# Optimization experiments

Hardware: AMD Instinct MI355X
Metric: run time of the kernel (lower is better)

## Reference

```python
import jax, jax.numpy as jnp
import numpy as np

IN_SIZE = 64
OUT_SIZE = 64
H1 = 2
H2 = 2
BATCH = 8192


def setup_inputs() -> dict:
    key = jax.random.key(0)
    ks = jax.random.split(key, 8)
    x = jax.random.normal(ks[0], (BATCH, IN_SIZE), dtype=jnp.float32)
    # Per-connection tiny MLP params; grid of (In, Out) subnets.
    # Layer 1: Linear(1, H1) -> w1:[In,Out,H1], b1:[In,Out,H1]
    # Layer 2: Linear(H1, H2) -> w2:[In,Out,H2,H1], b2:[In,Out,H2]
    # Layer 3: Linear(H2, 1) -> w3:[In,Out,H2], b3:[In,Out]
    s1 = 1.0  # kaiming-ish scale for fan_in=1
    s2 = 1.0 / np.sqrt(H1)
    s3 = 1.0 / np.sqrt(H2)
    w1 = jax.random.uniform(ks[1], (IN_SIZE, OUT_SIZE, H1), jnp.float32, -s1, s1)
    b1 = jax.random.uniform(ks[2], (IN_SIZE, OUT_SIZE, H1), jnp.float32, -s1, s1)
    w2 = jax.random.uniform(ks[3], (IN_SIZE, OUT_SIZE, H2, H1), jnp.float32, -s2, s2)
    b2 = jax.random.uniform(ks[4], (IN_SIZE, OUT_SIZE, H2), jnp.float32, -s2, s2)
    w3 = jax.random.uniform(ks[5], (IN_SIZE, OUT_SIZE, H2), jnp.float32, -s3, s3)
    b3 = jax.random.uniform(ks[6], (IN_SIZE, OUT_SIZE), jnp.float32, -s3, s3)
    return {"x": x, "w1": w1, "b1": b1, "w2": w2, "b2": b2, "w3": w3, "b3": b3}


def reference(x, w1, b1, w2, b2, w3, b3):
    # x: [B, In]. Each (in, out) connection has its own tiny 3-layer MLP on a scalar.
    # h1: [B, In, Out, H1] = relu(x * w1 + b1)  (input dim is 1, so it's a scale)
    h1 = jax.nn.relu(x[:, :, None, None] * w1[None] + b1[None])
    # h2: [B, In, Out, H2]
    h2 = jax.nn.relu(jnp.einsum('bioh,iokh->biok', h1, w2) + b2[None])
    # scalar output per connection: [B, In, Out]
    y = jnp.einsum('biok,iok->bio', h2, w3) + b3[None]
    # KAN combination: sum contributions over inputs -> [B, Out]
    return jnp.sum(y, axis=1)
```

## Files before the change

kernel.cpp:

```cpp
#include <hip/hip_runtime.h>


#define IN_SIZE  64
#define OUT_SIZE 64
#define BATCH    8192

constexpr int WAVES   = 16;
constexpr int I_CHUNK = 4;
constexpr int BT      = 32;
constexpr int RG      = 8;
constexpr int PAD     = 17;

__device__ __forceinline__ void pin(float& v) {
    asm volatile("" : "+v"(v));
}

__device__ __forceinline__ void conn(float xv, float2 W1, float2 B1,
                                     float4 W2, float2 B2, float2 W3,
                                     float& s) {
    const float h0 = fmaxf(fmaf(xv, W1.x, B1.x), 0.f);
    const float h1 = fmaxf(fmaf(xv, W1.y, B1.y), 0.f);
    float u0 = fmaf(h1, W2.y, fmaf(h0, W2.x, B2.x));
    float u1 = fmaf(h1, W2.w, fmaf(h0, W2.z, B2.y));
    u0 = fmaxf(u0, 0.f);
    u1 = fmaxf(u1, 0.f);
    s = fmaf(u0, W3.x, s);
    s = fmaf(u1, W3.y, s);
}

__global__ __launch_bounds__(1024, 4) void kan_kernel(
    const float* __restrict__ x,
    const float* __restrict__ w1, const float* __restrict__ b1,
    const float* __restrict__ w2, const float* __restrict__ b2,
    const float* __restrict__ w3, const float* __restrict__ b3,
    float* __restrict__ out)
{
    const int tid   = threadIdx.x;
    const int o     = tid & 63;
    const int wv    = tid >> 6;
    const int brow0 = blockIdx.x * BT;

    __shared__ float xs[BT * IN_SIZE];
    __shared__ float ps[RG * OUT_SIZE * PAD];

    {
        const float2* xg = reinterpret_cast<const float2*>(x + brow0 * IN_SIZE);
        reinterpret_cast<float2*>(xs)[tid] = xg[tid];
    }

    const int i0 = wv * I_CHUNK;
    float2 W1[I_CHUNK], B1[I_CHUNK], B2[I_CHUNK], W3[I_CHUNK];
    float4 W2[I_CHUNK];
    float bacc = 0.f;
    #pragma unroll
    for (int ic = 0; ic < I_CHUNK; ++ic) {
        const int base = (i0 + ic) * OUT_SIZE + o;
        W1[ic] = reinterpret_cast<const float2*>(w1)[base];
        B1[ic] = reinterpret_cast<const float2*>(b1)[base];
        W2[ic] = reinterpret_cast<const float4*>(w2)[base];
        B2[ic] = reinterpret_cast<const float2*>(b2)[base];
        W3[ic] = reinterpret_cast<const float2*>(w3)[base];
        bacc  += b3[base];
    }
    #pragma unroll
    for (int ic = 0; ic < I_CHUNK; ++ic) {
        pin(W1[ic].x); pin(W1[ic].y);  pin(B1[ic].x); pin(B1[ic].y);
        pin(W2[ic].x); pin(W2[ic].y);  pin(W2[ic].z); pin(W2[ic].w);
        pin(B2[ic].x); pin(B2[ic].y);  pin(W3[ic].x); pin(W3[ic].y);
    }

    __syncthreads();

    #pragma unroll
    for (int g = 0; g < BT / RG; ++g) {
        #pragma unroll
        for (int rr = 0; rr < RG; ++rr) {
            const int r = g * RG + rr;
            const float4 xa = *reinterpret_cast<const float4*>(xs + r * IN_SIZE + i0);
            float s = bacc;
            conn(xa.x, W1[0], B1[0], W2[0], B2[0], W3[0], s);
            conn(xa.y, W1[1], B1[1], W2[1], B2[1], W3[1], s);
            conn(xa.z, W1[2], B1[2], W2[2], B2[2], W3[2], s);
            conn(xa.w, W1[3], B1[3], W2[3], B2[3], W3[3], s);
            ps[(rr * OUT_SIZE + o) * PAD + wv] = s;
        }
        __syncthreads();

        if (tid < RG * OUT_SIZE) {
            const float* p = ps + tid * PAD;
            const float v = (((p[0]  + p[1])  + (p[2]  + p[3]))
                          +  ((p[4]  + p[5])  + (p[6]  + p[7])))
                          + (((p[8]  + p[9])  + (p[10] + p[11]))
                          +  ((p[12] + p[13]) + (p[14] + p[15])));
            out[(brow0 + g * RG) * OUT_SIZE + tid] = v;
        }
        __syncthreads();
    }
}

extern "C" void kernel_launch(void* const* d_in, const int* in_sizes, int n_in,
                              void* d_out, int out_size, void* d_ws, size_t ws_size,
                              hipStream_t stream) {
    const float* x  = (const float*)d_in[0];
    const float* w1 = (const float*)d_in[1];
    const float* b1 = (const float*)d_in[2];
    const float* w2 = (const float*)d_in[3];
    const float* b2 = (const float*)d_in[4];
    const float* w3 = (const float*)d_in[5];
    const float* b3 = (const float*)d_in[6];
    float* out = (float*)d_out;

    const int grid = BATCH / BT;
    kan_kernel<<<grid, 1024, 0, stream>>>(x, w1, b1, w2, b2, w3, b3, out);
}
```

Before: 17.11 us.

## Read x directly from global and reduce partial sums once per block

Drops the shared-memory staging of x; each wave loads its float4 slice of x straight from global memory, with the wave index made uniform via readfirstlane so the address is scalar. Partial sums for all 32 rows are written into a larger [waves][rows][out] shared buffer and reduced in a single pass after one barrier. This replaces the four grouped compute/reduce phases and their eight barriers. The cost is a larger shared buffer (128 KB), which limits occupancy to about one block per CU, and the min-blocks launch bound is removed.

```diff
diff --git a/kernel.cpp b/kernel.cpp
--- a/kernel.cpp
+++ b/kernel.cpp
@@ -8,8 +8,6 @@
 constexpr int WAVES   = 16;
 constexpr int I_CHUNK = 4;
 constexpr int BT      = 32;
-constexpr int RG      = 8;
-constexpr int PAD     = 17;
 
 __device__ __forceinline__ void pin(float& v) {
     asm volatile("" : "+v"(v));
@@ -28,7 +26,7 @@
     s = fmaf(u1, W3.y, s);
 }
 
-__global__ __launch_bounds__(1024, 4) void kan_kernel(
+__global__ __launch_bounds__(1024) void kan_kernel(
     const float* __restrict__ x,
     const float* __restrict__ w1, const float* __restrict__ b1,
     const float* __restrict__ w2, const float* __restrict__ b2,
@@ -37,16 +35,10 @@
 {
     const int tid   = threadIdx.x;
     const int o     = tid & 63;
-    const int wv    = tid >> 6;
+    const int wv    = __builtin_amdgcn_readfirstlane(tid >> 6);
     const int brow0 = blockIdx.x * BT;
 
-    __shared__ float xs[BT * IN_SIZE];
-    __shared__ float ps[RG * OUT_SIZE * PAD];
-
-    {
-        const float2* xg = reinterpret_cast<const float2*>(x + brow0 * IN_SIZE);
-        reinterpret_cast<float2*>(xs)[tid] = xg[tid];
-    }
+    __shared__ float ps[WAVES][BT][OUT_SIZE];
 
     const int i0 = wv * I_CHUNK;
     float2 W1[I_CHUNK], B1[I_CHUNK], B2[I_CHUNK], W3[I_CHUNK];
@@ -69,32 +61,27 @@
         pin(B2[ic].x); pin(B2[ic].y);  pin(W3[ic].x); pin(W3[ic].y);
     }
 
+    const float* xrow = x + brow0 * IN_SIZE + i0;
+    #pragma unroll 8
+    for (int r = 0; r < BT; ++r) {
+        const float4 xa = *reinterpret_cast<const float4*>(xrow + r * IN_SIZE);
+        float s = bacc;
+        conn(xa.x, W1[0], B1[0], W2[0], B2[0], W3[0], s);
+        conn(xa.y, W1[1], B1[1], W2[1], B2[1], W3[1], s);
+        conn(xa.z, W1[2], B1[2], W2[2], B2[2], W3[2], s);
+        conn(xa.w, W1[3], B1[3], W2[3], B2[3], W3[3], s);
+        ps[wv][r][o] = s;
+    }
+
     __syncthreads();
 
     #pragma unroll
-    for (int g = 0; g < BT / RG; ++g) {
+    for (int t = tid; t < BT * OUT_SIZE; t += 1024) {
+        const int r = t >> 6, oo = t & 63;
+        float v = 0.f;
         #pragma unroll
-        for (int rr = 0; rr < RG; ++rr) {
-            const int r = g * RG + rr;
-            const float4 xa = *reinterpret_cast<const float4*>(xs + r * IN_SIZE + i0);
-            float s = bacc;
-            conn(xa.x, W1[0], B1[0], W2[0], B2[0], W3[0], s);
-            conn(xa.y, W1[1], B1[1], W2[1], B2[1], W3[1], s);
-            conn(xa.z, W1[2], B1[2], W2[2], B2[2], W3[2], s);
-            conn(xa.w, W1[3], B1[3], W2[3], B2[3], W3[3], s);
-            ps[(rr * OUT_SIZE + o) * PAD + wv] = s;
-        }
-        __syncthreads();
-
-        if (tid < RG * OUT_SIZE) {
-            const float* p = ps + tid * PAD;
-            const float v = (((p[0]  + p[1])  + (p[2]  + p[3]))
-                          +  ((p[4]  + p[5])  + (p[6]  + p[7])))
-                          + (((p[8]  + p[9])  + (p[10] + p[11]))
-                          +  ((p[12] + p[13]) + (p[14] + p[15])));
-            out[(brow0 + g * RG) * OUT_SIZE + tid] = v;
-        }
-        __syncthreads();
+        for (int w = 0; w < WAVES; ++w) v += ps[w][r][oo];
+        out[brow0 * OUT_SIZE + t] = v;
     }
 }
 
```

Result: slower. 17.85 us (+4.3%).
